# Optimization experiments

Measured on AMD Instinct MI355X. Metric: run time of the kernel, lower is better.

## Reference

```python
import jax, jax.numpy as jnp
import numpy as np

B = 16384
OBS = 568        # 36 self features + 19 * 28 other-agent features
H = 256          # hidden_dim
SELF_DIM = 36
OTHER_DIM = 28
N_OTHER = (OBS - SELF_DIM) // OTHER_DIM  # 19


def _linear_init(key, fan_in, fan_out):
    # torch nn.Linear default: U(-1/sqrt(fan_in), 1/sqrt(fan_in))
    kw, kb = jax.random.split(key)
    s = 1.0 / np.sqrt(fan_in)
    W = jax.random.uniform(kw, (fan_in, fan_out), jnp.float32, -s, s)
    b = jax.random.uniform(kb, (fan_out,), jnp.float32, -s, s)
    return W, b


def setup_inputs() -> dict:
    key = jax.random.key(0)
    ks = jax.random.split(key, 10)
    x = jax.random.normal(ks[0], (B, OBS), jnp.float32)
    eps = jax.random.normal(ks[1], (B, H), jnp.float32)
    W_mu, b_mu = _linear_init(ks[2], OBS, H)
    W_var, b_var = _linear_init(ks[3], OBS, H)
    W_self, b_self = _linear_init(ks[4], SELF_DIM, H)
    W_other, b_other = _linear_init(ks[5], OTHER_DIM, H)
    W_q, b_q = _linear_init(ks[6], H, H)
    W_k, b_k = _linear_init(ks[7], H, H)
    W_v, b_v = _linear_init(ks[8], 2 * H, H)
    W_a, b_a = _linear_init(ks[9], 2 * H, H)
    return {"x": x, "eps": eps,
            "W_mu": W_mu, "b_mu": b_mu, "W_var": W_var, "b_var": b_var,
            "W_self": W_self, "b_self": b_self, "W_other": W_other, "b_other": b_other,
            "W_q": W_q, "b_q": b_q, "W_k": W_k, "b_k": b_k,
            "W_v": W_v, "b_v": b_v, "W_a": W_a, "b_a": b_a}


def reference(x, eps, W_mu, b_mu, W_var, b_var, W_self, b_self,
              W_other, b_other, W_q, b_q, W_k, b_k, W_v, b_v, W_a, b_a):
    relu = jax.nn.relu
    # VAE reparameterization (detach=False path)
    mu = x @ W_mu + b_mu                                  # [B, H]
    log_var = x @ W_var + b_var                           # [B, H]
    z = eps * jnp.exp(0.5 * log_var) + mu                 # [B, H]

    self_info = x[:, :SELF_DIM]                           # [B, 36]
    agents_info = x[:, SELF_DIM:].reshape(B, N_OTHER, OTHER_DIM)  # [B, N, 28]

    self_em = relu(self_info @ W_self + b_self)           # [B, H]
    other_ems = relu(agents_info @ W_other + b_other)     # [B, N, H]

    q = relu(z @ W_q + b_q)                               # [B, H]
    k = relu(other_ems @ W_k + b_k)                       # [B, N, H]
    v_in = jnp.concatenate(
        [other_ems, jnp.broadcast_to(self_em[:, None, :], (B, N_OTHER, H))], axis=-1)
    v = relu(v_in @ W_v + b_v)                            # [B, N, H]

    scores = jnp.einsum('bh,bnh->bn', q, k) / np.sqrt(H)  # [B, N]
    att_weight = jax.nn.softmax(scores, axis=-1)          # [B, N]
    h = jnp.einsum('bn,bnh->bh', att_weight, v)           # [B, H]

    out = relu(jnp.concatenate([h, self_em], axis=-1) @ W_a + b_a)  # [B, H]
    return out, att_weight[:, None, :]                    # att: [B, 1, N]
```

## Files before the change

kernel.cpp:

```cpp
#include <hip/hip_runtime.h>

typedef __bf16 bf16;
typedef __bf16 bf16x4 __attribute__((ext_vector_type(4)));
typedef __bf16 bf16x8 __attribute__((ext_vector_type(8)));
typedef float  f32x4  __attribute__((ext_vector_type(4)));

#define NB    16384
#define NOBS  568
#define NH    256
#define NAG   19

#define OFF_WT_MU    0u
#define OFF_WT_VAR   294912u
#define OFF_WT_SELF  589824u
#define OFF_WT_OTHER 622592u
#define OFF_WT_Q     638976u
#define OFF_WT_K     770048u
#define OFF_WT_V1    901120u
#define OFF_WT_V2    1032192u
#define OFF_WT_A1    1163264u
#define OFF_WT_A2    1294336u
#define OFF_Z        1425408u
#define OFF_SELF     9814016u
#define OFF_Q        18202624u
#define OFF_SV       26591232u
#define OFF_H        34979840u

static __device__ __forceinline__ unsigned short bfbits(float v) {
  bf16 b = (bf16)v;
  union { bf16 b; unsigned short u; } cvt; cvt.b = b; return cvt.u;
}

__global__ __launch_bounds__(256) void wprep(
    const float* __restrict__ Wmu, const float* __restrict__ Wvar,
    const float* __restrict__ Wself, const float* __restrict__ Wother,
    const float* __restrict__ Wq, const float* __restrict__ Wk,
    const float* __restrict__ Wv, const float* __restrict__ Wa, char* wsb)
{
  const float* src; bf16* dst; int K, Kp; bool chunked = false;
  switch (blockIdx.y) {
    case 0: src = Wmu;        dst = (bf16*)(wsb + OFF_WT_MU);    K = 568; Kp = 576; break;
    case 1: src = Wvar;       dst = (bf16*)(wsb + OFF_WT_VAR);   K = 568; Kp = 576; break;
    case 2: src = Wself;      dst = (bf16*)(wsb + OFF_WT_SELF);  K = 36;  Kp = 64;  break;
    case 3: src = Wother;     dst = (bf16*)(wsb + OFF_WT_OTHER); K = 28;  Kp = 32;  break;
    case 4: src = Wq;         dst = (bf16*)(wsb + OFF_WT_Q);     K = 256; Kp = 256; break;
    case 5: src = Wk;         dst = (bf16*)(wsb + OFF_WT_K);     K = 256; Kp = 256; chunked = true; break;
    case 6: src = Wv;         dst = (bf16*)(wsb + OFF_WT_V1);    K = 256; Kp = 256; chunked = true; break;
    case 7: src = Wv + 65536; dst = (bf16*)(wsb + OFF_WT_V2);    K = 256; Kp = 256; break;
    case 8: src = Wa;         dst = (bf16*)(wsb + OFF_WT_A1);    K = 256; Kp = 256; break;
    default: src = Wa + 65536; dst = (bf16*)(wsb + OFF_WT_A2);   K = 256; Kp = 256; break;
  }
  int total = 256 * Kp;
  if (chunked) {
    for (int i = blockIdx.x * 256 + threadIdx.x; i < total; i += gridDim.x * 256) {
      int ch = i >> 13, n = (i >> 5) & 255, kk = i & 31;
      int k = ch * 32 + kk;
      dst[i] = (bf16)src[k * 256 + n];
    }
  } else {
    for (int i = blockIdx.x * 256 + threadIdx.x; i < total; i += gridDim.x * 256) {
      int n = i / Kp, k = i - n * Kp;
      dst[i] = (k < K) ? (bf16)src[k * 256 + n] : (bf16)0.f;
    }
  }
}

__global__ __launch_bounds__(256, 3) void gemm_zself(
    const float* __restrict__ x,
    const bf16* __restrict__ WtMu, const bf16* __restrict__ WtVar,
    const bf16* __restrict__ WtSelf,
    const float* __restrict__ b_mu, const float* __restrict__ b_var,
    const float* __restrict__ b_self, const float* __restrict__ eps,
    bf16* __restrict__ zout, bf16* __restrict__ selfout)
{
  __shared__ bf16 ldsA[64 * 40];
  __shared__ bf16 ldsB[128 * 40];
  __shared__ bf16 ldsB2[128 * 40];

  const int tid = threadIdx.x;
  const int wave = tid >> 6;
  const int lane = tid & 63;
  const int quad = lane >> 4;
  const int m = lane & 15;
  const int rowbase = blockIdx.x * 64;
  const int colbase = (blockIdx.y & 1) * 128;
  const bool isZ = blockIdx.y < 2;
  const int K = isZ ? 576 : 64;
  const bf16* __restrict__ Wt = isZ ? WtMu : WtSelf;
  const float* __restrict__ bias = isZ ? b_mu : b_self;

  f32x4 acc[8], accB[8];
  const f32x4 z4 = {0.f, 0.f, 0.f, 0.f};
#pragma unroll
  for (int ct = 0; ct < 8; ++ct) { acc[ct] = z4; accB[ct] = z4; }

  for (int kc = 0; kc < K; kc += 32) {
    __syncthreads();
    {
#pragma unroll
      for (int it = 0; it < 2; ++it) {
        int p = tid + 256 * it;
        int r = p >> 3, fs = p & 7;
        int k = kc + fs * 4;
        const float* src = x + (size_t)(rowbase + r) * 568 + k;
        float v0, v1, v2, v3;
        if (k + 4 <= 568) {
          float4 v = *(const float4*)src;
          v0 = v.x; v1 = v.y; v2 = v.z; v3 = v.w;
        } else {
          v0 = (k + 0 < 568) ? src[0] : 0.f;
          v1 = (k + 1 < 568) ? src[1] : 0.f;
          v2 = (k + 2 < 568) ? src[2] : 0.f;
          v3 = (k + 3 < 568) ? src[3] : 0.f;
        }
        bf16x4 o = {(bf16)v0, (bf16)v1, (bf16)v2, (bf16)v3};
        *(bf16x4*)(ldsA + r * 40 + fs * 4) = o;
      }
    }
#pragma unroll
    for (int it = 0; it < 2; ++it) {
      int p = tid + 256 * it;
      int n = p >> 2, f = p & 3;
      *(bf16x8*)(ldsB + n * 40 + f * 8) =
          *(const bf16x8*)(Wt + (size_t)(colbase + n) * K + kc + f * 8);
    }
    if (isZ) {
#pragma unroll
      for (int it = 0; it < 2; ++it) {
        int p = tid + 256 * it;
        int n = p >> 2, f = p & 3;
        *(bf16x8*)(ldsB2 + n * 40 + f * 8) =
            *(const bf16x8*)(WtVar + (size_t)(colbase + n) * 576 + kc + f * 8);
      }
    }
    __syncthreads();
    bf16x8 afrag = *(const bf16x8*)(ldsA + (wave * 16 + m) * 40 + quad * 8);
#pragma unroll
    for (int ct = 0; ct < 8; ++ct) {
      bf16x8 bfrag = *(const bf16x8*)(ldsB + (ct * 16 + m) * 40 + quad * 8);
      acc[ct] = __builtin_amdgcn_mfma_f32_16x16x32_bf16(afrag, bfrag, acc[ct], 0, 0, 0);
      if (isZ) {
        bf16x8 b2 = *(const bf16x8*)(ldsB2 + (ct * 16 + m) * 40 + quad * 8);
        accB[ct] = __builtin_amdgcn_mfma_f32_16x16x32_bf16(afrag, b2, accB[ct], 0, 0, 0);
      }
    }
  }
#pragma unroll
  for (int ct = 0; ct < 8; ++ct) {
    const int col = colbase + ct * 16 + m;
    const float bv = bias[col];
#pragma unroll
    for (int r = 0; r < 4; ++r) {
      const size_t row = (size_t)rowbase + wave * 16 + quad * 4 + r;
      float v = acc[ct][r] + bv;
      if (isZ) {
        float lv = accB[ct][r] + b_var[col];
        float zz = eps[row * 256 + col] * __expf(0.5f * lv) + v;
        zout[row * 256 + col] = (bf16)zz;
      } else {
        selfout[row * 256 + col] = (bf16)(v > 0.f ? v : 0.f);
      }
    }
  }
}

__global__ __launch_bounds__(256, 4) void gemm_qsv(
    const bf16* __restrict__ zb, const bf16* __restrict__ selfb,
    const bf16* __restrict__ WtQ, const bf16* __restrict__ WtV2,
    const float* __restrict__ b_q, const float* __restrict__ b_v,
    bf16* __restrict__ qout, bf16* __restrict__ svout)
{
  __shared__ bf16 ldsA[64 * 40];
  __shared__ bf16 ldsB[128 * 40];

  const int tid = threadIdx.x;
  const int wave = tid >> 6;
  const int lane = tid & 63;
  const int quad = lane >> 4;
  const int m = lane & 15;
  const int rowbase = blockIdx.x * 64;
  const int colbase = (blockIdx.y & 1) * 128;
  const bool isQ = blockIdx.y < 2;
  const bf16* __restrict__ Ap = isQ ? zb : selfb;
  const bf16* __restrict__ Wt = isQ ? WtQ : WtV2;
  const float* __restrict__ bias = isQ ? b_q : b_v;
  bf16* __restrict__ outp = isQ ? qout : svout;

  f32x4 acc[8];
  const f32x4 z4 = {0.f, 0.f, 0.f, 0.f};
#pragma unroll
  for (int ct = 0; ct < 8; ++ct) acc[ct] = z4;

  for (int kc = 0; kc < 256; kc += 32) {
    __syncthreads();
    {
      int p = tid;
      int r = p >> 2, f = p & 3;
      *(bf16x8*)(ldsA + r * 40 + f * 8) =
          *(const bf16x8*)(Ap + (size_t)(rowbase + r) * 256 + kc + f * 8);
    }
#pragma unroll
    for (int it = 0; it < 2; ++it) {
      int p = tid + 256 * it;
      int n = p >> 2, f = p & 3;
      *(bf16x8*)(ldsB + n * 40 + f * 8) =
          *(const bf16x8*)(Wt + (size_t)(colbase + n) * 256 + kc + f * 8);
    }
    __syncthreads();
    bf16x8 afrag = *(const bf16x8*)(ldsA + (wave * 16 + m) * 40 + quad * 8);
#pragma unroll
    for (int ct = 0; ct < 8; ++ct) {
      bf16x8 bfrag = *(const bf16x8*)(ldsB + (ct * 16 + m) * 40 + quad * 8);
      acc[ct] = __builtin_amdgcn_mfma_f32_16x16x32_bf16(afrag, bfrag, acc[ct], 0, 0, 0);
    }
  }
#pragma unroll
  for (int ct = 0; ct < 8; ++ct) {
    const int col = colbase + ct * 16 + m;
    const float bv = bias[col];
#pragma unroll
    for (int r = 0; r < 4; ++r) {
      const size_t row = (size_t)rowbase + wave * 16 + quad * 4 + r;
      float v = acc[ct][r] + bv;
      if (isQ) v = (v > 0.f ? v : 0.f);
      outp[row * 256 + col] = (bf16)v;
    }
  }
}

template<bool UNUSED>
__global__ __launch_bounds__(256, 2) void gemm_dualA(
    const bf16* __restrict__ A1, const bf16* __restrict__ A2,
    const bf16* __restrict__ Wt1, const bf16* __restrict__ Wt2,
    const float* __restrict__ bias, float* __restrict__ outp)
{
  __shared__ bf16 ldsA[64 * 40];
  __shared__ bf16 ldsB[128 * 40];

  const int tid = threadIdx.x;
  const int wave = tid >> 6;
  const int lane = tid & 63;
  const int quad = lane >> 4;
  const int m = lane & 15;
  const int rowbase = blockIdx.x * 64;
  const int colbase = blockIdx.y * 128;

  f32x4 acc[8];
  const f32x4 z4 = {0.f, 0.f, 0.f, 0.f};
#pragma unroll
  for (int ct = 0; ct < 8; ++ct) acc[ct] = z4;

  for (int pass = 0; pass < 2; ++pass) {
    const bf16* Ap = (pass == 0) ? A1 : A2;
    const bf16* Wp = (pass == 0) ? Wt1 : Wt2;
    for (int kc = 0; kc < 256; kc += 32) {
      __syncthreads();
      {
        int p = tid;
        int r = p >> 2, f = p & 3;
        *(bf16x8*)(ldsA + r * 40 + f * 8) =
            *(const bf16x8*)(Ap + (size_t)(rowbase + r) * 256 + kc + f * 8);
      }
#pragma unroll
      for (int it = 0; it < 2; ++it) {
        int p = tid + 256 * it;
        int n = p >> 2, f = p & 3;
        *(bf16x8*)(ldsB + n * 40 + f * 8) =
            *(const bf16x8*)(Wp + (size_t)(colbase + n) * 256 + kc + f * 8);
      }
      __syncthreads();
      bf16x8 afrag = *(const bf16x8*)(ldsA + (wave * 16 + m) * 40 + quad * 8);
#pragma unroll
      for (int ct = 0; ct < 8; ++ct) {
        bf16x8 bfrag = *(const bf16x8*)(ldsB + (ct * 16 + m) * 40 + quad * 8);
        acc[ct] = __builtin_amdgcn_mfma_f32_16x16x32_bf16(afrag, bfrag, acc[ct], 0, 0, 0);
      }
    }
  }
#pragma unroll
  for (int ct = 0; ct < 8; ++ct) {
    const int col = colbase + ct * 16 + m;
    const float bv = bias[col];
#pragma unroll
    for (int r = 0; r < 4; ++r) {
      const size_t row = (size_t)rowbase + wave * 16 + quad * 4 + r;
      float v = acc[ct][r] + bv;
      outp[row * 256 + col] = (v > 0.f ? v : 0.f);
    }
  }
}

__global__ __launch_bounds__(512, 4) void k_fused(
    const float* __restrict__ x, const bf16* __restrict__ qb,
    const bf16* __restrict__ svb,
    const bf16* __restrict__ WtOther, const float* __restrict__ b_other,
    const bf16* __restrict__ WtKc, const float* __restrict__ b_k,
    const bf16* __restrict__ WtVc,
    float* __restrict__ att_out, bf16* __restrict__ hb)
{
  __shared__ bf16 ldsO[80 * 264];
  __shared__ bf16 ldsA1[80 * 40];
  __shared__ bf16 qh16[1024];
  __shared__ bf16 svl16[1024];
  float* spart = (float*)ldsA1;
  float* attl  = (float*)ldsA1 + 320;

  const int tid = threadIdx.x, wave = tid >> 6, lane = tid & 63;
  const int quad = lane >> 4, m = lane & 15;
  const int b0 = blockIdx.x * 4;
  const int kvw = wave & 3;
  const bool isV = wave >= 4;

  ((unsigned*)qh16)[tid]  = ((const unsigned*)(qb  + (size_t)b0 * 256))[tid];
  ((unsigned*)svl16)[tid] = ((const unsigned*)(svb + (size_t)b0 * 256))[tid];
  for (int i = tid; i < 80 * 16; i += 512) {
    int r = i >> 4, kk = (i & 15) * 2;
    int n = r >> 2, bb = r & 3;
    float v0 = 0.f, v1 = 0.f;
    if (n < 19) {
      const float* base = x + (size_t)(b0 + bb) * NOBS + 36 + n * 28;
      if (kk < 28) v0 = base[kk];
      if (kk + 1 < 28) v1 = base[kk + 1];
    }
    unsigned u0 = bfbits(v0), u1 = bfbits(v1);
    *(unsigned*)(ldsA1 + r * 40 + kk) = u0 | (u1 << 16);
  }

  const f32x4 z4 = {0.f, 0.f, 0.f, 0.f};

  const bf16* __restrict__ Bc = isV ? WtVc : WtKc;
  const int cb = (kvw * 64 + m) * 32 + quad * 8;
  bf16x8 bE[4];
#pragma unroll
  for (int c = 0; c < 4; ++c) bE[c] = *(const bf16x8*)(Bc + cb + c * 512);

  __syncthreads();

  {
    float bo[2];
    bf16x8 bfr[2];
#pragma unroll
    for (int c = 0; c < 2; ++c) {
      int col = (2 * wave + c) * 16 + m;
      bo[c] = b_other[col];
      bfr[c] = *(const bf16x8*)(WtOther + col * 32 + quad * 8);
    }
    f32x4 acc1[5][2];
#pragma unroll
    for (int rt = 0; rt < 5; ++rt) {
      bf16x8 a = *(const bf16x8*)(ldsA1 + (rt * 16 + m) * 40 + quad * 8);
#pragma unroll
      for (int c = 0; c < 2; ++c)
        acc1[rt][c] = __builtin_amdgcn_mfma_f32_16x16x32_bf16(a, bfr[c], z4, 0, 0, 0);
    }
#pragma unroll
    for (int rt = 0; rt < 5; ++rt)
#pragma unroll
      for (int c = 0; c < 2; ++c) {
        int col = (2 * wave + c) * 16 + m;
#pragma unroll
        for (int r = 0; r < 4; ++r) {
          float v = acc1[rt][c][r] + bo[c];
          v = v > 0.f ? v : 0.f;
          unsigned u = bfbits(v);
          unsigned other = (unsigned)__shfl_xor((int)u, 1, 64);
          if ((m & 1) == 0) {
            int rowl = rt * 16 + quad * 4 + r;
            *(unsigned*)(ldsO + rowl * 264 + col) = u | (other << 16);
          }
        }
      }
  }
  __syncthreads();

  f32x4 acc[5][4];
#pragma unroll
  for (int rt = 0; rt < 5; ++rt)
#pragma unroll
    for (int c = 0; c < 4; ++c) acc[rt][c] = z4;

  {
#pragma unroll 1
    for (int ch = 0; ch < 8; ch += 2) {
      bf16x8 bO[4];
#pragma unroll
      for (int c = 0; c < 4; ++c)
        bO[c] = *(const bf16x8*)(Bc + (size_t)(ch + 1) * 8192 + cb + c * 512);
      const int kc0 = ch * 32;
#pragma unroll
      for (int rt = 0; rt < 5; ++rt) {
        bf16x8 a = *(const bf16x8*)(ldsO + (rt * 16 + m) * 264 + kc0 + quad * 8);
#pragma unroll
        for (int c = 0; c < 4; ++c)
          acc[rt][c] = __builtin_amdgcn_mfma_f32_16x16x32_bf16(a, bE[c], acc[rt][c], 0, 0, 0);
      }
#pragma unroll
      for (int c = 0; c < 4; ++c)
        bE[c] = *(const bf16x8*)(Bc + (size_t)(ch + 2) * 8192 + cb + c * 512);
      const int kc1 = kc0 + 32;
#pragma unroll
      for (int rt = 0; rt < 5; ++rt) {
        bf16x8 a = *(const bf16x8*)(ldsO + (rt * 16 + m) * 264 + kc1 + quad * 8);
#pragma unroll
        for (int c = 0; c < 4; ++c)
          acc[rt][c] = __builtin_amdgcn_mfma_f32_16x16x32_bf16(a, bO[c], acc[rt][c], 0, 0, 0);
      }
    }
  }

  if (!isV) {
    float qreg[4][4], bkreg[4];
#pragma unroll
    for (int c = 0; c < 4; ++c) {
      int col = (4 * wave + c) * 16 + m;
      bkreg[c] = b_k[col];
#pragma unroll
      for (int r = 0; r < 4; ++r) qreg[c][r] = (float)qh16[r * 256 + col];
    }
#pragma unroll
    for (int rt = 0; rt < 5; ++rt) {
      float part[4] = {0.f, 0.f, 0.f, 0.f};
#pragma unroll
      for (int c = 0; c < 4; ++c) {
#pragma unroll
        for (int r = 0; r < 4; ++r) {
          float kv = acc[rt][c][r] + bkreg[c];
          kv = kv > 0.f ? kv : 0.f;
          part[r] += kv * qreg[c][r];
        }
      }
#pragma unroll
      for (int r = 0; r < 4; ++r) {
        float p = part[r];
        p += __shfl_xor(p, 1, 64);
        p += __shfl_xor(p, 2, 64);
        p += __shfl_xor(p, 4, 64);
        p += __shfl_xor(p, 8, 64);
        if (m == 0) spart[wave * 80 + rt * 16 + quad * 4 + r] = p;
      }
    }
  }
  __syncthreads();

  if (!isV && lane < 32) {
    const int bb = wave, j = lane;
    float s = -1e30f;
    if (j < 19) {
      int row = j * 4 + bb;
      s = (spart[row] + spart[80 + row] + spart[160 + row] + spart[240 + row]) * 0.0625f;
    }
    float mx = s;
#pragma unroll
    for (int off = 16; off >= 1; off >>= 1) mx = fmaxf(mx, __shfl_xor(mx, off, 32));
    float e = (j < 19) ? __expf(s - mx) : 0.f;
    float sum = e;
#pragma unroll
    for (int off = 16; off >= 1; off >>= 1) sum += __shfl_xor(sum, off, 32);
    float inv = 1.f / sum;
    float a = e * inv;
    if (j < 20) attl[j * 4 + bb] = a;
    if (j < 19) att_out[(size_t)(b0 + bb) * 19 + j] = a;
  }
  __syncthreads();

  if (isV) {
    float svreg[4][4];
#pragma unroll
    for (int c = 0; c < 4; ++c) {
      int col = (4 * kvw + c) * 16 + m;
#pragma unroll
      for (int r = 0; r < 4; ++r) svreg[c][r] = (float)svl16[r * 256 + col];
    }
    float hacc[4][4];
#pragma unroll
    for (int c = 0; c < 4; ++c)
#pragma unroll
      for (int r = 0; r < 4; ++r) hacc[c][r] = 0.f;
#pragma unroll
    for (int rt = 0; rt < 5; ++rt) {
      float av[4];
#pragma unroll
      for (int r = 0; r < 4; ++r) av[r] = attl[rt * 16 + quad * 4 + r];
#pragma unroll
      for (int c = 0; c < 4; ++c) {
#pragma unroll
        for (int r = 0; r < 4; ++r) {
          float v = acc[rt][c][r] + svreg[c][r];
          v = v > 0.f ? v : 0.f;
          hacc[c][r] += v * av[r];
        }
      }
    }
#pragma unroll
    for (int c = 0; c < 4; ++c)
#pragma unroll
      for (int r = 0; r < 4; ++r) {
        float h = hacc[c][r];
        h += __shfl_xor(h, 16, 64);
        h += __shfl_xor(h, 32, 64);
        if (quad == 0) qh16[r * 256 + (4 * kvw + c) * 16 + m] = (bf16)h;
      }
  }
  __syncthreads();
  ((unsigned*)(hb + (size_t)b0 * 256))[tid] = ((const unsigned*)qh16)[tid];
}

extern "C" void kernel_launch(void* const* d_in, const int* in_sizes, int n_in,
                              void* d_out, int out_size, void* d_ws, size_t ws_size,
                              hipStream_t stream) {
  (void)in_sizes; (void)n_in; (void)out_size; (void)ws_size;
  const float* x      = (const float*)d_in[0];
  const float* eps    = (const float*)d_in[1];
  const float* W_mu   = (const float*)d_in[2];
  const float* b_mu   = (const float*)d_in[3];
  const float* W_var  = (const float*)d_in[4];
  const float* b_var  = (const float*)d_in[5];
  const float* W_self = (const float*)d_in[6];
  const float* b_self = (const float*)d_in[7];
  const float* W_other= (const float*)d_in[8];
  const float* b_other= (const float*)d_in[9];
  const float* W_q    = (const float*)d_in[10];
  const float* b_q    = (const float*)d_in[11];
  const float* W_k    = (const float*)d_in[12];
  const float* b_k    = (const float*)d_in[13];
  const float* W_v    = (const float*)d_in[14];
  const float* b_v    = (const float*)d_in[15];
  const float* W_a    = (const float*)d_in[16];
  const float* b_a    = (const float*)d_in[17];

  char* wsb = (char*)d_ws;
  bf16* WtMu    = (bf16*)(wsb + OFF_WT_MU);
  bf16* WtVar   = (bf16*)(wsb + OFF_WT_VAR);
  bf16* WtSelf  = (bf16*)(wsb + OFF_WT_SELF);
  bf16* WtOther = (bf16*)(wsb + OFF_WT_OTHER);
  bf16* WtQ     = (bf16*)(wsb + OFF_WT_Q);
  bf16* WtK     = (bf16*)(wsb + OFF_WT_K);
  bf16* WtV1    = (bf16*)(wsb + OFF_WT_V1);
  bf16* WtV2    = (bf16*)(wsb + OFF_WT_V2);
  bf16* WtA1    = (bf16*)(wsb + OFF_WT_A1);
  bf16* WtA2    = (bf16*)(wsb + OFF_WT_A2);
  bf16* zbuf    = (bf16*)(wsb + OFF_Z);
  bf16* selfbuf = (bf16*)(wsb + OFF_SELF);
  bf16* qbuf    = (bf16*)(wsb + OFF_Q);
  bf16* svbuf   = (bf16*)(wsb + OFF_SV);
  bf16* hbuf    = (bf16*)(wsb + OFF_H);

  float* out = (float*)d_out;
  float* att_out = out + (size_t)NB * 256;

  dim3 blk(256);
  wprep<<<dim3(160, 10), blk, 0, stream>>>(W_mu, W_var, W_self, W_other, W_q, W_k, W_v, W_a, wsb);
  gemm_zself<<<dim3(NB / 64, 4), blk, 0, stream>>>(x, WtMu, WtVar, WtSelf,
                                                   b_mu, b_var, b_self, eps, zbuf, selfbuf);
  gemm_qsv<<<dim3(NB / 64, 4), blk, 0, stream>>>(zbuf, selfbuf, WtQ, WtV2,
                                                 b_q, b_v, qbuf, svbuf);
  k_fused<<<NB / 4, dim3(512), 0, stream>>>(x, qbuf, svbuf, WtOther, b_other, WtK, b_k,
                                            WtV1, att_out, hbuf);
  gemm_dualA<true><<<dim3(NB / 64, 2), blk, 0, stream>>>(hbuf, selfbuf, WtA1, WtA2, b_a, out);
}
```

Before: 338.2 us.

## Fuse z/self and q/sv GEMMs into one kernel keeping z in LDS

Merges the two front GEMM kernels into a single gemm_front kernel in which each block computes all 256 columns for 64 rows: first mu/logvar (or self_em), then reparameterizes z into LDS and immediately multiplies by W_q (or W_v2). Weights are now stored in a 32-wide k-chunked layout and read directly from global/L2 into registers with software double-buffering instead of being staged through LDS. This removes the z round-trip to global memory and one launch, and packs bf16 outputs into 32-bit stores via lane shuffles. In exchange each block does much more work with a larger register footprint (32 accumulators plus 32 prefetched B fragments), and the grid shrinks to 512 blocks, which lowers occupancy and parallelism.

```diff
diff --git a/kernel.cpp b/kernel.cpp
--- a/kernel.cpp
+++ b/kernel.cpp
@@ -37,25 +37,25 @@
     const float* __restrict__ Wq, const float* __restrict__ Wk,
     const float* __restrict__ Wv, const float* __restrict__ Wa, char* wsb)
 {
-  const float* src; bf16* dst; int K, Kp; bool chunked = false;
+  const float* src; bf16* dst; int K, Kp; bool chunked = true;
   switch (blockIdx.y) {
     case 0: src = Wmu;        dst = (bf16*)(wsb + OFF_WT_MU);    K = 568; Kp = 576; break;
     case 1: src = Wvar;       dst = (bf16*)(wsb + OFF_WT_VAR);   K = 568; Kp = 576; break;
     case 2: src = Wself;      dst = (bf16*)(wsb + OFF_WT_SELF);  K = 36;  Kp = 64;  break;
     case 3: src = Wother;     dst = (bf16*)(wsb + OFF_WT_OTHER); K = 28;  Kp = 32;  break;
     case 4: src = Wq;         dst = (bf16*)(wsb + OFF_WT_Q);     K = 256; Kp = 256; break;
-    case 5: src = Wk;         dst = (bf16*)(wsb + OFF_WT_K);     K = 256; Kp = 256; chunked = true; break;
-    case 6: src = Wv;         dst = (bf16*)(wsb + OFF_WT_V1);    K = 256; Kp = 256; chunked = true; break;
+    case 5: src = Wk;         dst = (bf16*)(wsb + OFF_WT_K);     K = 256; Kp = 256; break;
+    case 6: src = Wv;         dst = (bf16*)(wsb + OFF_WT_V1);    K = 256; Kp = 256; break;
     case 7: src = Wv + 65536; dst = (bf16*)(wsb + OFF_WT_V2);    K = 256; Kp = 256; break;
-    case 8: src = Wa;         dst = (bf16*)(wsb + OFF_WT_A1);    K = 256; Kp = 256; break;
-    default: src = Wa + 65536; dst = (bf16*)(wsb + OFF_WT_A2);   K = 256; Kp = 256; break;
+    case 8: src = Wa;         dst = (bf16*)(wsb + OFF_WT_A1);    K = 256; Kp = 256; chunked = false; break;
+    default: src = Wa + 65536; dst = (bf16*)(wsb + OFF_WT_A2);   K = 256; Kp = 256; chunked = false; break;
   }
   int total = 256 * Kp;
   if (chunked) {
     for (int i = blockIdx.x * 256 + threadIdx.x; i < total; i += gridDim.x * 256) {
       int ch = i >> 13, n = (i >> 5) & 255, kk = i & 31;
       int k = ch * 32 + kk;
-      dst[i] = (bf16)src[k * 256 + n];
+      dst[i] = (k < K) ? (bf16)src[k * 256 + n] : (bf16)0.f;
     }
   } else {
     for (int i = blockIdx.x * 256 + threadIdx.x; i < total; i += gridDim.x * 256) {
@@ -65,165 +65,132 @@
   }
 }
 
-__global__ __launch_bounds__(256, 3) void gemm_zself(
+__global__ __launch_bounds__(256, 2) void gemm_front(
     const float* __restrict__ x,
     const bf16* __restrict__ WtMu, const bf16* __restrict__ WtVar,
     const bf16* __restrict__ WtSelf,
+    const bf16* __restrict__ WtQc, const bf16* __restrict__ WtV2c,
     const float* __restrict__ b_mu, const float* __restrict__ b_var,
-    const float* __restrict__ b_self, const float* __restrict__ eps,
-    bf16* __restrict__ zout, bf16* __restrict__ selfout)
+    const float* __restrict__ b_self,
+    const float* __restrict__ b_q, const float* __restrict__ b_v,
+    const float* __restrict__ eps,
+    bf16* __restrict__ qout, bf16* __restrict__ selfout, bf16* __restrict__ svout)
 {
-  __shared__ bf16 ldsA[64 * 40];
-  __shared__ bf16 ldsB[128 * 40];
-  __shared__ bf16 ldsB2[128 * 40];
+  __shared__ bf16 zl[64 * 264];
 
   const int tid = threadIdx.x;
   const int wave = tid >> 6;
   const int lane = tid & 63;
   const int quad = lane >> 4;
   const int m = lane & 15;
-  const int rowbase = blockIdx.x * 64;
-  const int colbase = (blockIdx.y & 1) * 128;
-  const bool isZ = blockIdx.y < 2;
-  const int K = isZ ? 576 : 64;
-  const bf16* __restrict__ Wt = isZ ? WtMu : WtSelf;
-  const float* __restrict__ bias = isZ ? b_mu : b_self;
-
-  f32x4 acc[8], accB[8];
+  const bool isZ = !(blockIdx.x & 1);
+  const int rowbase = (blockIdx.x >> 1) * 64;
+
   const f32x4 z4 = {0.f, 0.f, 0.f, 0.f};
-#pragma unroll
-  for (int ct = 0; ct < 8; ++ct) { acc[ct] = z4; accB[ct] = z4; }
-
-  for (int kc = 0; kc < K; kc += 32) {
-    __syncthreads();
-    {
-#pragma unroll
-      for (int it = 0; it < 2; ++it) {
-        int p = tid + 256 * it;
-        int r = p >> 3, fs = p & 7;
-        int k = kc + fs * 4;
-        const float* src = x + (size_t)(rowbase + r) * 568 + k;
-        float v0, v1, v2, v3;
-        if (k + 4 <= 568) {
-          float4 v = *(const float4*)src;
-          v0 = v.x; v1 = v.y; v2 = v.z; v3 = v.w;
-        } else {
-          v0 = (k + 0 < 568) ? src[0] : 0.f;
-          v1 = (k + 1 < 568) ? src[1] : 0.f;
-          v2 = (k + 2 < 568) ? src[2] : 0.f;
-          v3 = (k + 3 < 568) ? src[3] : 0.f;
-        }
-        bf16x4 o = {(bf16)v0, (bf16)v1, (bf16)v2, (bf16)v3};
-        *(bf16x4*)(ldsA + r * 40 + fs * 4) = o;
-      }
-    }
-#pragma unroll
-    for (int it = 0; it < 2; ++it) {
-      int p = tid + 256 * it;
-      int n = p >> 2, f = p & 3;
-      *(bf16x8*)(ldsB + n * 40 + f * 8) =
-          *(const bf16x8*)(Wt + (size_t)(colbase + n) * K + kc + f * 8);
+  f32x4 a1[16], a2[16];
+#pragma unroll
+  for (int ct = 0; ct < 16; ++ct) { a1[ct] = z4; a2[ct] = z4; }
+
+  const int KA = isZ ? 576 : 64;
+  const bf16* __restrict__ W1 = isZ ? WtMu : WtSelf;
+
+  for (int ch = 0; ch < KA / 32; ++ch) {
+    const int kc = ch * 32;
+    bf16x8 af;
+    if (kc + quad * 8 < 568) {
+      const float* ap = x + (size_t)(rowbase + wave * 16 + m) * 568 + kc + quad * 8;
+      float4 f0 = *(const float4*)ap;
+      float4 f1 = *(const float4*)(ap + 4);
+      af[0] = (bf16)f0.x; af[1] = (bf16)f0.y; af[2] = (bf16)f0.z; af[3] = (bf16)f0.w;
+      af[4] = (bf16)f1.x; af[5] = (bf16)f1.y; af[6] = (bf16)f1.z; af[7] = (bf16)f1.w;
+    } else {
+#pragma unroll
+      for (int e = 0; e < 8; ++e) af[e] = (bf16)0.f;
+    }
+    const bf16* bp1 = W1 + (size_t)ch * 8192 + m * 32 + quad * 8;
+#pragma unroll
+    for (int ct = 0; ct < 16; ++ct) {
+      bf16x8 b1 = *(const bf16x8*)(bp1 + ct * 512);
+      a1[ct] = __builtin_amdgcn_mfma_f32_16x16x32_bf16(af, b1, a1[ct], 0, 0, 0);
     }
     if (isZ) {
-#pragma unroll
-      for (int it = 0; it < 2; ++it) {
-        int p = tid + 256 * it;
-        int n = p >> 2, f = p & 3;
-        *(bf16x8*)(ldsB2 + n * 40 + f * 8) =
-            *(const bf16x8*)(WtVar + (size_t)(colbase + n) * 576 + kc + f * 8);
-      }
-    }
-    __syncthreads();
-    bf16x8 afrag = *(const bf16x8*)(ldsA + (wave * 16 + m) * 40 + quad * 8);
-#pragma unroll
-    for (int ct = 0; ct < 8; ++ct) {
-      bf16x8 bfrag = *(const bf16x8*)(ldsB + (ct * 16 + m) * 40 + quad * 8);
-      acc[ct] = __builtin_amdgcn_mfma_f32_16x16x32_bf16(afrag, bfrag, acc[ct], 0, 0, 0);
+      const bf16* bp2 = WtVar + (size_t)ch * 8192 + m * 32 + quad * 8;
+#pragma unroll
+      for (int ct = 0; ct < 16; ++ct) {
+        bf16x8 b2 = *(const bf16x8*)(bp2 + ct * 512);
+        a2[ct] = __builtin_amdgcn_mfma_f32_16x16x32_bf16(af, b2, a2[ct], 0, 0, 0);
+      }
+    }
+  }
+
+#pragma unroll
+  for (int ct = 0; ct < 16; ++ct) {
+    const int col = ct * 16 + m;
+    const float bv1 = isZ ? b_mu[col] : b_self[col];
+    const float bv2 = isZ ? b_var[col] : 0.f;
+#pragma unroll
+    for (int r = 0; r < 4; ++r) {
+      const int rowl = wave * 16 + quad * 4 + r;
+      const size_t row = (size_t)rowbase + rowl;
+      float v;
       if (isZ) {
-        bf16x8 b2 = *(const bf16x8*)(ldsB2 + (ct * 16 + m) * 40 + quad * 8);
-        accB[ct] = __builtin_amdgcn_mfma_f32_16x16x32_bf16(afrag, b2, accB[ct], 0, 0, 0);
-      }
-    }
-  }
-#pragma unroll
-  for (int ct = 0; ct < 8; ++ct) {
-    const int col = colbase + ct * 16 + m;
-    const float bv = bias[col];
+        float mu = a1[ct][r] + bv1;
+        float lv = a2[ct][r] + bv2;
+        v = eps[row * 256 + col] * __expf(0.5f * lv) + mu;
+      } else {
+        v = a1[ct][r] + bv1;
+        v = v > 0.f ? v : 0.f;
+      }
+      unsigned u = bfbits(v);
+      unsigned other = (unsigned)__shfl_xor((int)u, 1, 64);
+      if ((m & 1) == 0) {
+        unsigned pk = u | (other << 16);
+        *(unsigned*)(zl + rowl * 264 + col) = pk;
+        if (!isZ) *(unsigned*)(selfout + row * 256 + col) = pk;
+      }
+    }
+  }
+
+#pragma unroll
+  for (int ct = 0; ct < 16; ++ct) a1[ct] = z4;
+  const bf16* __restrict__ W3 = isZ ? WtQc : WtV2c;
+  const int cb2 = m * 32 + quad * 8;
+  bf16x8 pA[16], pB[16];
+#pragma unroll
+  for (int ct = 0; ct < 16; ++ct) pA[ct] = *(const bf16x8*)(W3 + cb2 + ct * 512);
+#pragma unroll 1
+  for (int ch2 = 0; ch2 < 8; ch2 += 2) {
+#pragma unroll
+    for (int ct = 0; ct < 16; ++ct)
+      pB[ct] = *(const bf16x8*)(W3 + (size_t)(ch2 + 1) * 8192 + cb2 + ct * 512);
+    bf16x8 af0 = *(const bf16x8*)(zl + (wave * 16 + m) * 264 + ch2 * 32 + quad * 8);
+#pragma unroll
+    for (int ct = 0; ct < 16; ++ct)
+      a1[ct] = __builtin_amdgcn_mfma_f32_16x16x32_bf16(af0, pA[ct], a1[ct], 0, 0, 0);
+#pragma unroll
+    for (int ct = 0; ct < 16; ++ct)
+      pA[ct] = *(const bf16x8*)(W3 + (size_t)(ch2 + 2) * 8192 + cb2 + ct * 512);
+    bf16x8 af1 = *(const bf16x8*)(zl + (wave * 16 + m) * 264 + (ch2 + 1) * 32 + quad * 8);
+#pragma unroll
+    for (int ct = 0; ct < 16; ++ct)
+      a1[ct] = __builtin_amdgcn_mfma_f32_16x16x32_bf16(af1, pB[ct], a1[ct], 0, 0, 0);
+  }
+
+  const float* __restrict__ b3 = isZ ? b_q : b_v;
+  bf16* __restrict__ out3 = isZ ? qout : svout;
+#pragma unroll
+  for (int ct = 0; ct < 16; ++ct) {
+    const int col = ct * 16 + m;
+    const float bv = b3[col];
 #pragma unroll
     for (int r = 0; r < 4; ++r) {
       const size_t row = (size_t)rowbase + wave * 16 + quad * 4 + r;
-      float v = acc[ct][r] + bv;
-      if (isZ) {
-        float lv = accB[ct][r] + b_var[col];
-        float zz = eps[row * 256 + col] * __expf(0.5f * lv) + v;
-        zout[row * 256 + col] = (bf16)zz;
-      } else {
-        selfout[row * 256 + col] = (bf16)(v > 0.f ? v : 0.f);
-      }
-    }
-  }
-}
-
-__global__ __launch_bounds__(256, 4) void gemm_qsv(
-    const bf16* __restrict__ zb, const bf16* __restrict__ selfb,
-    const bf16* __restrict__ WtQ, const bf16* __restrict__ WtV2,
-    const float* __restrict__ b_q, const float* __restrict__ b_v,
-    bf16* __restrict__ qout, bf16* __restrict__ svout)
-{
-  __shared__ bf16 ldsA[64 * 40];
-  __shared__ bf16 ldsB[128 * 40];
-
-  const int tid = threadIdx.x;
-  const int wave = tid >> 6;
-  const int lane = tid & 63;
-  const int quad = lane >> 4;
-  const int m = lane & 15;
-  const int rowbase = blockIdx.x * 64;
-  const int colbase = (blockIdx.y & 1) * 128;
-  const bool isQ = blockIdx.y < 2;
-  const bf16* __restrict__ Ap = isQ ? zb : selfb;
-  const bf16* __restrict__ Wt = isQ ? WtQ : WtV2;
-  const float* __restrict__ bias = isQ ? b_q : b_v;
-  bf16* __restrict__ outp = isQ ? qout : svout;
-
-  f32x4 acc[8];
-  const f32x4 z4 = {0.f, 0.f, 0.f, 0.f};
-#pragma unroll
-  for (int ct = 0; ct < 8; ++ct) acc[ct] = z4;
-
-  for (int kc = 0; kc < 256; kc += 32) {
-    __syncthreads();
-    {
-      int p = tid;
-      int r = p >> 2, f = p & 3;
-      *(bf16x8*)(ldsA + r * 40 + f * 8) =
-          *(const bf16x8*)(Ap + (size_t)(rowbase + r) * 256 + kc + f * 8);
-    }
-#pragma unroll
-    for (int it = 0; it < 2; ++it) {
-      int p = tid + 256 * it;
-      int n = p >> 2, f = p & 3;
-      *(bf16x8*)(ldsB + n * 40 + f * 8) =
-          *(const bf16x8*)(Wt + (size_t)(colbase + n) * 256 + kc + f * 8);
-    }
-    __syncthreads();
-    bf16x8 afrag = *(const bf16x8*)(ldsA + (wave * 16 + m) * 40 + quad * 8);
-#pragma unroll
-    for (int ct = 0; ct < 8; ++ct) {
-      bf16x8 bfrag = *(const bf16x8*)(ldsB + (ct * 16 + m) * 40 + quad * 8);
-      acc[ct] = __builtin_amdgcn_mfma_f32_16x16x32_bf16(afrag, bfrag, acc[ct], 0, 0, 0);
-    }
-  }
-#pragma unroll
-  for (int ct = 0; ct < 8; ++ct) {
-    const int col = colbase + ct * 16 + m;
-    const float bv = bias[col];
-#pragma unroll
-    for (int r = 0; r < 4; ++r) {
-      const size_t row = (size_t)rowbase + wave * 16 + quad * 4 + r;
-      float v = acc[ct][r] + bv;
-      if (isQ) v = (v > 0.f ? v : 0.f);
-      outp[row * 256 + col] = (bf16)v;
+      float v = a1[ct][r] + bv;
+      if (isZ) v = v > 0.f ? v : 0.f;
+      unsigned u = bfbits(v);
+      unsigned other = (unsigned)__shfl_xor((int)u, 1, 64);
+      if ((m & 1) == 0)
+        *(unsigned*)(out3 + row * 256 + col) = u | (other << 16);
     }
   }
 }
@@ -539,7 +506,6 @@
   bf16* WtV2    = (bf16*)(wsb + OFF_WT_V2);
   bf16* WtA1    = (bf16*)(wsb + OFF_WT_A1);
   bf16* WtA2    = (bf16*)(wsb + OFF_WT_A2);
-  bf16* zbuf    = (bf16*)(wsb + OFF_Z);
   bf16* selfbuf = (bf16*)(wsb + OFF_SELF);
   bf16* qbuf    = (bf16*)(wsb + OFF_Q);
   bf16* svbuf   = (bf16*)(wsb + OFF_SV);
@@ -550,10 +516,9 @@
 
   dim3 blk(256);
   wprep<<<dim3(160, 10), blk, 0, stream>>>(W_mu, W_var, W_self, W_other, W_q, W_k, W_v, W_a, wsb);
-  gemm_zself<<<dim3(NB / 64, 4), blk, 0, stream>>>(x, WtMu, WtVar, WtSelf,
-                                                   b_mu, b_var, b_self, eps, zbuf, selfbuf);
-  gemm_qsv<<<dim3(NB / 64, 4), blk, 0, stream>>>(zbuf, selfbuf, WtQ, WtV2,
-                                                 b_q, b_v, qbuf, svbuf);
+  gemm_front<<<512, blk, 0, stream>>>(x, WtMu, WtVar, WtSelf, WtQ, WtV2,
+                                      b_mu, b_var, b_self, b_q, b_v, eps,
+                                      qbuf, selfbuf, svbuf);
   k_fused<<<NB / 4, dim3(512), 0, stream>>>(x, qbuf, svbuf, WtOther, b_other, WtK, b_k,
                                             WtV1, att_out, hbuf);
   gemm_dualA<true><<<dim3(NB / 64, 2), blk, 0, stream>>>(hbuf, selfbuf, WtA1, WtA2, b_a, out);
```

Measured after the change: 387.9 us. 14.7% more time.

## Double-buffer q/sv and output GEMMs with direct global-to-LDS loads

Applied to the files above, without the earlier changes.

Rewrites gemm_qsv and gemm_dualA to stage A and B tiles straight into LDS with global_load_lds, double-buffering so the next K-chunk loads while MFMAs run on the current one. It drops one barrier per iteration. The weight prep now writes Wq, Wv2 and Wa in the chunked (32-wide K block) layout so B tiles are contiguous 16-byte copies. It also raises gemm_dualA's occupancy hint from 2 to 4. In exchange, the unpadded LDS rows (stride 32) may cause bank conflicts on the fragment reads, and correctness relies on the lane-ordered LDS placement of global_load_lds matching the tile layout.

```diff
diff --git a/kernel.cpp b/kernel.cpp
--- a/kernel.cpp
+++ b/kernel.cpp
@@ -31,6 +31,12 @@
   union { bf16 b; unsigned short u; } cvt; cvt.b = b; return cvt.u;
 }
 
+static __device__ __forceinline__ void gload16(const bf16* g, bf16* l) {
+  __builtin_amdgcn_global_load_lds(
+      (const __attribute__((address_space(1))) void*)g,
+      (__attribute__((address_space(3))) void*)(void*)l, 16, 0, 0);
+}
+
 __global__ __launch_bounds__(256) void wprep(
     const float* __restrict__ Wmu, const float* __restrict__ Wvar,
     const float* __restrict__ Wself, const float* __restrict__ Wother,
@@ -43,12 +49,12 @@
     case 1: src = Wvar;       dst = (bf16*)(wsb + OFF_WT_VAR);   K = 568; Kp = 576; break;
     case 2: src = Wself;      dst = (bf16*)(wsb + OFF_WT_SELF);  K = 36;  Kp = 64;  break;
     case 3: src = Wother;     dst = (bf16*)(wsb + OFF_WT_OTHER); K = 28;  Kp = 32;  break;
-    case 4: src = Wq;         dst = (bf16*)(wsb + OFF_WT_Q);     K = 256; Kp = 256; break;
+    case 4: src = Wq;         dst = (bf16*)(wsb + OFF_WT_Q);     K = 256; Kp = 256; chunked = true; break;
     case 5: src = Wk;         dst = (bf16*)(wsb + OFF_WT_K);     K = 256; Kp = 256; chunked = true; break;
     case 6: src = Wv;         dst = (bf16*)(wsb + OFF_WT_V1);    K = 256; Kp = 256; chunked = true; break;
-    case 7: src = Wv + 65536; dst = (bf16*)(wsb + OFF_WT_V2);    K = 256; Kp = 256; break;
-    case 8: src = Wa;         dst = (bf16*)(wsb + OFF_WT_A1);    K = 256; Kp = 256; break;
-    default: src = Wa + 65536; dst = (bf16*)(wsb + OFF_WT_A2);   K = 256; Kp = 256; break;
+    case 7: src = Wv + 65536; dst = (bf16*)(wsb + OFF_WT_V2);    K = 256; Kp = 256; chunked = true; break;
+    case 8: src = Wa;         dst = (bf16*)(wsb + OFF_WT_A1);    K = 256; Kp = 256; chunked = true; break;
+    default: src = Wa + 65536; dst = (bf16*)(wsb + OFF_WT_A2);   K = 256; Kp = 256; chunked = true; break;
   }
   int total = 256 * Kp;
   if (chunked) {
@@ -166,12 +172,12 @@
 
 __global__ __launch_bounds__(256, 4) void gemm_qsv(
     const bf16* __restrict__ zb, const bf16* __restrict__ selfb,
-    const bf16* __restrict__ WtQ, const bf16* __restrict__ WtV2,
+    const bf16* __restrict__ WtQc, const bf16* __restrict__ WtV2c,
     const float* __restrict__ b_q, const float* __restrict__ b_v,
     bf16* __restrict__ qout, bf16* __restrict__ svout)
 {
-  __shared__ bf16 ldsA[64 * 40];
-  __shared__ bf16 ldsB[128 * 40];
+  __shared__ __align__(16) bf16 lA[2][64 * 32];
+  __shared__ __align__(16) bf16 lB[2][128 * 32];
 
   const int tid = threadIdx.x;
   const int wave = tid >> 6;
@@ -182,7 +188,7 @@
   const int colbase = (blockIdx.y & 1) * 128;
   const bool isQ = blockIdx.y < 2;
   const bf16* __restrict__ Ap = isQ ? zb : selfb;
-  const bf16* __restrict__ Wt = isQ ? WtQ : WtV2;
+  const bf16* __restrict__ Wc = isQ ? WtQc : WtV2c;
   const float* __restrict__ bias = isQ ? b_q : b_v;
   bf16* __restrict__ outp = isQ ? qout : svout;
 
@@ -191,29 +197,33 @@
 #pragma unroll
   for (int ct = 0; ct < 8; ++ct) acc[ct] = z4;
 
-  for (int kc = 0; kc < 256; kc += 32) {
+  const size_t arow = (size_t)(rowbase + (tid >> 2)) * 256 + (tid & 3) * 8;
+  const size_t bbase = (size_t)colbase * 32 + (size_t)tid * 8;
+
+  gload16(Ap + arow, &lA[0][wave * 512]);
+  gload16(Wc + bbase, &lB[0][wave * 512]);
+  gload16(Wc + bbase + 2048, &lB[0][2048 + wave * 512]);
+  __syncthreads();
+
+#pragma unroll
+  for (int ch = 0; ch < 8; ++ch) {
+    const int cur = ch & 1;
+    if (ch < 7) {
+      const int nxt = cur ^ 1;
+      const size_t cof = (size_t)(ch + 1) * 8192;
+      gload16(Ap + arow + (ch + 1) * 32, &lA[nxt][wave * 512]);
+      gload16(Wc + cof + bbase, &lB[nxt][wave * 512]);
+      gload16(Wc + cof + bbase + 2048, &lB[nxt][2048 + wave * 512]);
+    }
+    bf16x8 afrag = *(const bf16x8*)(&lA[cur][(wave * 16 + m) * 32 + quad * 8]);
+#pragma unroll
+    for (int ct = 0; ct < 8; ++ct) {
+      bf16x8 bfrag = *(const bf16x8*)(&lB[cur][(ct * 16 + m) * 32 + quad * 8]);
+      acc[ct] = __builtin_amdgcn_mfma_f32_16x16x32_bf16(afrag, bfrag, acc[ct], 0, 0, 0);
+    }
     __syncthreads();
-    {
-      int p = tid;
-      int r = p >> 2, f = p & 3;
-      *(bf16x8*)(ldsA + r * 40 + f * 8) =
-          *(const bf16x8*)(Ap + (size_t)(rowbase + r) * 256 + kc + f * 8);
-    }
-#pragma unroll
-    for (int it = 0; it < 2; ++it) {
-      int p = tid + 256 * it;
-      int n = p >> 2, f = p & 3;
-      *(bf16x8*)(ldsB + n * 40 + f * 8) =
-          *(const bf16x8*)(Wt + (size_t)(colbase + n) * 256 + kc + f * 8);
-    }
-    __syncthreads();
-    bf16x8 afrag = *(const bf16x8*)(ldsA + (wave * 16 + m) * 40 + quad * 8);
-#pragma unroll
-    for (int ct = 0; ct < 8; ++ct) {
-      bf16x8 bfrag = *(const bf16x8*)(ldsB + (ct * 16 + m) * 40 + quad * 8);
-      acc[ct] = __builtin_amdgcn_mfma_f32_16x16x32_bf16(afrag, bfrag, acc[ct], 0, 0, 0);
-    }
-  }
+  }
+
 #pragma unroll
   for (int ct = 0; ct < 8; ++ct) {
     const int col = colbase + ct * 16 + m;
@@ -228,14 +238,13 @@
   }
 }
 
-template<bool UNUSED>
-__global__ __launch_bounds__(256, 2) void gemm_dualA(
+__global__ __launch_bounds__(256, 4) void gemm_dualA(
     const bf16* __restrict__ A1, const bf16* __restrict__ A2,
-    const bf16* __restrict__ Wt1, const bf16* __restrict__ Wt2,
+    const bf16* __restrict__ Wt1c, const bf16* __restrict__ Wt2c,
     const float* __restrict__ bias, float* __restrict__ outp)
 {
-  __shared__ bf16 ldsA[64 * 40];
-  __shared__ bf16 ldsB[128 * 40];
+  __shared__ __align__(16) bf16 lA[2][64 * 32];
+  __shared__ __align__(16) bf16 lB[2][128 * 32];
 
   const int tid = threadIdx.x;
   const int wave = tid >> 6;
@@ -250,33 +259,35 @@
 #pragma unroll
   for (int ct = 0; ct < 8; ++ct) acc[ct] = z4;
 
-  for (int pass = 0; pass < 2; ++pass) {
-    const bf16* Ap = (pass == 0) ? A1 : A2;
-    const bf16* Wp = (pass == 0) ? Wt1 : Wt2;
-    for (int kc = 0; kc < 256; kc += 32) {
-      __syncthreads();
-      {
-        int p = tid;
-        int r = p >> 2, f = p & 3;
-        *(bf16x8*)(ldsA + r * 40 + f * 8) =
-            *(const bf16x8*)(Ap + (size_t)(rowbase + r) * 256 + kc + f * 8);
-      }
-#pragma unroll
-      for (int it = 0; it < 2; ++it) {
-        int p = tid + 256 * it;
-        int n = p >> 2, f = p & 3;
-        *(bf16x8*)(ldsB + n * 40 + f * 8) =
-            *(const bf16x8*)(Wp + (size_t)(colbase + n) * 256 + kc + f * 8);
-      }
-      __syncthreads();
-      bf16x8 afrag = *(const bf16x8*)(ldsA + (wave * 16 + m) * 40 + quad * 8);
-#pragma unroll
-      for (int ct = 0; ct < 8; ++ct) {
-        bf16x8 bfrag = *(const bf16x8*)(ldsB + (ct * 16 + m) * 40 + quad * 8);
-        acc[ct] = __builtin_amdgcn_mfma_f32_16x16x32_bf16(afrag, bfrag, acc[ct], 0, 0, 0);
-      }
-    }
-  }
+  const size_t arow = (size_t)(rowbase + (tid >> 2)) * 256 + (tid & 3) * 8;
+  const size_t bbase = (size_t)colbase * 32 + (size_t)tid * 8;
+
+  auto stageT = [&](int buf, int t) {
+    const int ch = t & 7;
+    const bf16* Astep = (t < 8) ? A1 : A2;
+    const bf16* Wstep = (t < 8) ? Wt1c : Wt2c;
+    const size_t cof = (size_t)ch * 8192;
+    gload16(Astep + arow + ch * 32, &lA[buf][wave * 512]);
+    gload16(Wstep + cof + bbase, &lB[buf][wave * 512]);
+    gload16(Wstep + cof + bbase + 2048, &lB[buf][2048 + wave * 512]);
+  };
+
+  stageT(0, 0);
+  __syncthreads();
+
+#pragma unroll
+  for (int t = 0; t < 16; ++t) {
+    const int cur = t & 1;
+    if (t < 15) stageT(cur ^ 1, t + 1);
+    bf16x8 afrag = *(const bf16x8*)(&lA[cur][(wave * 16 + m) * 32 + quad * 8]);
+#pragma unroll
+    for (int ct = 0; ct < 8; ++ct) {
+      bf16x8 bfrag = *(const bf16x8*)(&lB[cur][(ct * 16 + m) * 32 + quad * 8]);
+      acc[ct] = __builtin_amdgcn_mfma_f32_16x16x32_bf16(afrag, bfrag, acc[ct], 0, 0, 0);
+    }
+    __syncthreads();
+  }
+
 #pragma unroll
   for (int ct = 0; ct < 8; ++ct) {
     const int col = colbase + ct * 16 + m;
@@ -556,5 +567,5 @@
                                                  b_q, b_v, qbuf, svbuf);
   k_fused<<<NB / 4, dim3(512), 0, stream>>>(x, qbuf, svbuf, WtOther, b_other, WtK, b_k,
                                             WtV1, att_out, hbuf);
-  gemm_dualA<true><<<dim3(NB / 64, 2), blk, 0, stream>>>(hbuf, selfbuf, WtA1, WtA2, b_a, out);
-}
+  gemm_dualA<<<dim3(NB / 64, 2), blk, 0, stream>>>(hbuf, selfbuf, WtA1, WtA2, b_a, out);
+}
```

Measured after the change: 336.6 us. No clear change (-0.5%).
